# Performance work log

Measured on AMD Instinct MI355X. Metric: run time of the kernel, lower is better.

## Reference

```python
import jax, jax.numpy as jnp
import numpy as np

EMB = 2048
H = 16
Q_RANK = 1536
KV_RANK = 512
ROPE_D = 64
NOPE_D = 64
V_D = 128
QK_D = ROPE_D + NOPE_D  # 128
ROPE_BASE = 10000.0
SCALING = 1.0  # query_pre_attn_scalar ** -0.5 with scalar=1.0


def apply_rope(x):
    """torchtune-style interleaved RoPE. x: (B, S, H, D)."""
    S, D = x.shape[1], x.shape[-1]
    theta = 1.0 / (ROPE_BASE ** (jnp.arange(0, D, 2, dtype=jnp.float32) / D))  # (D/2,)
    ang = jnp.arange(S, dtype=jnp.float32)[:, None] * theta[None, :]  # (S, D/2)
    cos = jnp.cos(ang)[None, :, None, :]
    sin = jnp.sin(ang)[None, :, None, :]
    xf = x.astype(jnp.float32).reshape(*x.shape[:-1], D // 2, 2)
    x0, x1 = xf[..., 0], xf[..., 1]
    out = jnp.stack([x0 * cos - x1 * sin, x1 * cos + x0 * sin], axis=-1)
    return out.reshape(x.shape).astype(x.dtype)


def setup_inputs() -> dict:
    key = jax.random.key(0)
    ks = jax.random.split(key, 6)
    s = lambda fan_in: 1.0 / np.sqrt(fan_in)
    return {
        "x": jax.random.normal(ks[0], (2, 2048, EMB), dtype=jnp.float32),
        "q_a_w": jax.random.uniform(ks[1], (Q_RANK, EMB), jnp.float32, -s(EMB), s(EMB)),
        "q_b_w": jax.random.uniform(ks[2], (H * QK_D, Q_RANK), jnp.float32, -s(Q_RANK), s(Q_RANK)),
        "kv_a_w": jax.random.uniform(ks[3], (KV_RANK + ROPE_D, EMB), jnp.float32, -s(EMB), s(EMB)),
        "kv_b_w": jax.random.uniform(ks[4], (H * (NOPE_D + V_D), KV_RANK), jnp.float32, -s(KV_RANK), s(KV_RANK)),
        "o_w": jax.random.uniform(ks[5], (EMB, H * V_D), jnp.float32, -s(H * V_D), s(H * V_D)),
    }


def reference(x, q_a_w, q_b_w, kv_a_w, kv_b_w, o_w):
    B, S, _ = x.shape
    # LoRA-compressed Q projection
    q = (x @ q_a_w.T) @ q_b_w.T  # (B, S, H*QK_D)
    q = q.reshape(B, S, H, QK_D).transpose(0, 2, 1, 3)  # (B, H, S, QK_D)
    q_pass, q_rot = q[..., :NOPE_D], q[..., NOPE_D:]
    # Compressed KV with shared rope key
    ckv = x @ kv_a_w.T  # (B, S, KV_RANK + ROPE_D)
    k_pass_c, k_rot = ckv[..., :KV_RANK], ckv[..., KV_RANK:]
    kvb = (k_pass_c @ kv_b_w.T).reshape(B, S, H, NOPE_D + V_D).transpose(0, 2, 1, 3)
    k_pass, v = kvb[..., :NOPE_D], kvb[..., NOPE_D:]  # (B,H,S,NOPE_D), (B,H,S,V_D)
    # RoPE (applied in (B,S,H,D) layout, as in the original)
    q_rot = apply_rope(q_rot.transpose(0, 2, 1, 3)).transpose(0, 2, 1, 3)
    k_rot = apply_rope(k_rot[:, :, None, :])  # (B, S, 1, ROPE_D), shared across heads
    k_rot = jnp.broadcast_to(k_rot.transpose(0, 2, 1, 3), (B, H, S, ROPE_D))
    query = jnp.concatenate([q_pass, q_rot], axis=-1)  # (B, H, S, QK_D)
    key = jnp.concatenate([k_pass, k_rot], axis=-1)
    # NOTE: original passes attention_mask=None -> no causal mask applied.
    scores = jnp.einsum("bhqd,bhkd->bhqk", query, key) * SCALING
    attn = jax.nn.softmax(scores.astype(jnp.float32), axis=-1).astype(query.dtype)
    out = jnp.einsum("bhqk,bhkd->bhqd", attn, v)  # (B, H, S, V_D)
    out = out.transpose(0, 2, 1, 3).reshape(B, S, H * V_D)
    return out @ o_w.T
```

## Files before the change

### kernel.cpp

```cpp
#include <hip/hip_runtime.h>
#include <stdint.h>

#define EMB 2048
#define NH 16
#define QRANK 1536
#define KVRANK 512
#define ROPED 64
#define NOPED 64
#define VD 128
#define QKD 128
#define SEQ 2048
#define BATCH 2
#define BS 4096
#define BHD 32
#define NCOMB 2112
#define LOG2E 1.4426950408889634f

typedef __attribute__((ext_vector_type(4))) float f32x4;
typedef __attribute__((ext_vector_type(8))) short s16x8;
typedef __attribute__((ext_vector_type(4))) short s16x4;
typedef __attribute__((ext_vector_type(2))) unsigned int u32x2;

__device__ __forceinline__ float bf2f(unsigned short u) {
  return __uint_as_float(((unsigned int)u) << 16);
}
__device__ __forceinline__ unsigned short f2bf(float f) {
  unsigned int u = __float_as_uint(f);
  u += 0x7fff + ((u >> 16) & 1);
  return (unsigned short)(u >> 16);
}

__device__ __forceinline__ float vexp2(float x) {
#if __has_builtin(__builtin_amdgcn_exp2f)
  return __builtin_amdgcn_exp2f(x);
#else
  return exp2f(x);
#endif
}

__device__ __forceinline__ unsigned int pk_bf16_trunc(float e0, float e1) {
#if __has_builtin(__builtin_amdgcn_perm)
  return __builtin_amdgcn_perm(__float_as_uint(e1), __float_as_uint(e0), 0x07060302u);
#else
  return (__float_as_uint(e1) & 0xffff0000u) | (__float_as_uint(e0) >> 16);
#endif
}

__device__ __forceinline__ void pl32swap(unsigned int& a, unsigned int& b) {
#if __has_builtin(__builtin_amdgcn_permlane32_swap)
  u32x2 r = __builtin_amdgcn_permlane32_swap(a, b, false, false);
  a = r.x; b = r.y;
#else
  asm("v_permlane32_swap_b32 %0, %1" : "+v"(a), "+v"(b));
#endif
}
__device__ __forceinline__ void pl16swap(unsigned int& a, unsigned int& b) {
#if __has_builtin(__builtin_amdgcn_permlane16_swap)
  u32x2 r = __builtin_amdgcn_permlane16_swap(a, b, false, false);
  a = r.x; b = r.y;
#else
  asm("v_permlane16_swap_b32 %0, %1" : "+v"(a), "+v"(b));
#endif
}

__device__ __forceinline__ void gld_lds16(const unsigned short* g, unsigned short* l) {
  __builtin_amdgcn_global_load_lds((const __attribute__((address_space(1))) void*)g,
                                   (__attribute__((address_space(3))) void*)l,
                                   16, 0, 0);
}

#define N4_X   (BS * EMB / 4)
#define N4_QA  (QRANK * EMB / 4)
#define N4_KVA ((KVRANK + ROPED) * EMB / 4)
#define N4_QB  (NH * QKD * QRANK / 4)
#define N4_KVB (NH * 192 * KVRANK / 4)
#define N4_O   (EMB * NH * VD / 4)
#define N4_TOT (N4_X + N4_QA + N4_KVA + N4_QB + N4_KVB + N4_O)

__global__ void cast_all(const float* __restrict__ x, const float* __restrict__ qa,
                         const float* __restrict__ kva, const float* __restrict__ qb,
                         const float* __restrict__ kvb, const float* __restrict__ ow,
                         unsigned short* __restrict__ Xb, unsigned short* __restrict__ Wcomb,
                         unsigned short* __restrict__ Wqb, unsigned short* __restrict__ Wkvb,
                         unsigned short* __restrict__ Wo) {
  int i = blockIdx.x * blockDim.x + threadIdx.x;
  int stride = gridDim.x * blockDim.x;
  for (; i < N4_TOT; i += stride) {
    const float4* src;
    ushort4* dst;
    int j = i;
    if (j < N4_X) { src = (const float4*)x; dst = (ushort4*)Xb; }
    else if ((j -= N4_X) < N4_QA) { src = (const float4*)qa; dst = (ushort4*)Wcomb; }
    else if ((j -= N4_QA) < N4_KVA) { src = (const float4*)kva; dst = (ushort4*)(Wcomb + (size_t)QRANK * EMB); }
    else if ((j -= N4_KVA) < N4_QB) { src = (const float4*)qb; dst = (ushort4*)Wqb; }
    else if ((j -= N4_QB) < N4_KVB) { src = (const float4*)kvb; dst = (ushort4*)Wkvb; }
    else { j -= N4_KVB; src = (const float4*)ow; dst = (ushort4*)Wo; }
    float4 v = src[j];
    ushort4 o;
    o.x = f2bf(v.x); o.y = f2bf(v.y); o.z = f2bf(v.z); o.w = f2bf(v.w);
    dst[j] = o;
  }
}

template <int OUT_F32>
__global__ __launch_bounds__(256, 2) void gemm_bt(
    const unsigned short* __restrict__ A, int lda,
    const unsigned short* __restrict__ W, int ldw,
    void* __restrict__ C, int M, int N, int K)
{
  __shared__ __align__(16) unsigned short As[128 * 64];
  __shared__ __align__(16) unsigned short Ws[128 * 64];
  const int tid = threadIdx.x;
  const int wave = tid >> 6;
  const int lane = tid & 63;
  const int ln = lane & 15;
  const int quad = lane >> 4;
  const int bm = blockIdx.y * 128;
  const int bn = blockIdx.x * 128;
  const int wm = (wave >> 1) * 64;
  const int wn = (wave & 1) * 64;

  f32x4 acc[4][4] = {};

  const int rel8 = lane >> 3;
  const int csw = ((lane & 7) ^ rel8) * 8;

  for (int k0 = 0; k0 < K; k0 += 64) {
#pragma unroll
    for (int it = 0; it < 4; ++it) {
      int rb = wave * 32 + it * 8;
      gld_lds16(A + (size_t)(bm + rb + rel8) * lda + k0 + csw, &As[rb * 64]);
    }
#pragma unroll
    for (int it = 0; it < 4; ++it) {
      int rb = wave * 32 + it * 8;
      int wr = bn + rb + rel8;
      if (wr >= N) wr = N - 1;
      gld_lds16(W + (size_t)wr * ldw + k0 + csw, &Ws[rb * 64]);
    }
    __syncthreads();
#pragma unroll
    for (int kk = 0; kk < 64; kk += 32) {
      s16x8 a[4], b[4];
#pragma unroll
      for (int mt = 0; mt < 4; ++mt)
        a[mt] = *(const s16x8*)&As[(wm + mt * 16 + ln) * 64 + ((kk / 8 + quad) ^ (ln & 7)) * 8];
#pragma unroll
      for (int nt = 0; nt < 4; ++nt)
        b[nt] = *(const s16x8*)&Ws[(wn + nt * 16 + ln) * 64 + ((kk / 8 + quad) ^ (ln & 7)) * 8];
#pragma unroll
      for (int mt = 0; mt < 4; ++mt)
#pragma unroll
        for (int nt = 0; nt < 4; ++nt)
          acc[mt][nt] = __builtin_amdgcn_mfma_f32_16x16x32_bf16(a[mt], b[nt], acc[mt][nt], 0, 0, 0);
    }
    __syncthreads();
  }
#pragma unroll
  for (int mt = 0; mt < 4; ++mt) {
    int row = bm + wm + mt * 16 + quad * 4;
#pragma unroll
    for (int nt = 0; nt < 4; ++nt) {
      int col = bn + wn + nt * 16 + ln;
      if (col < N) {
#pragma unroll
        for (int r = 0; r < 4; ++r) {
          float v = acc[mt][nt][r];
          if (OUT_F32)
            ((float*)C)[(size_t)(row + r) * N + col] = v;
          else
            ((unsigned short*)C)[(size_t)(row + r) * N + col] = f2bf(v);
        }
      }
    }
  }
}

__global__ __launch_bounds__(256, 2) void gemm_q_rope(
    const unsigned short* __restrict__ A, int lda,
    const unsigned short* __restrict__ W, int ldw,
    unsigned short* __restrict__ Qry, int K)
{
  __shared__ __align__(16) unsigned short As[128 * 64];
  __shared__ __align__(16) unsigned short Ws[128 * 64];
  const int tid = threadIdx.x;
  const int wave = tid >> 6;
  const int lane = tid & 63;
  const int ln = lane & 15;
  const int quad = lane >> 4;
  const int bm = blockIdx.y * 128;
  const int bn = blockIdx.x * 128;
  const int wm = (wave >> 1) * 64;
  const int wn = (wave & 1) * 64;

  f32x4 acc[4][4] = {};
  const int rel8 = lane >> 3;
  const int csw = ((lane & 7) ^ rel8) * 8;

  for (int k0 = 0; k0 < K; k0 += 64) {
#pragma unroll
    for (int it = 0; it < 4; ++it) {
      int rb = wave * 32 + it * 8;
      gld_lds16(A + (size_t)(bm + rb + rel8) * lda + k0 + csw, &As[rb * 64]);
    }
#pragma unroll
    for (int it = 0; it < 4; ++it) {
      int rb = wave * 32 + it * 8;
      gld_lds16(W + (size_t)(bn + rb + rel8) * ldw + k0 + csw, &Ws[rb * 64]);
    }
    __syncthreads();
#pragma unroll
    for (int kk = 0; kk < 64; kk += 32) {
      s16x8 a[4], b[4];
#pragma unroll
      for (int mt = 0; mt < 4; ++mt)
        a[mt] = *(const s16x8*)&As[(wm + mt * 16 + ln) * 64 + ((kk / 8 + quad) ^ (ln & 7)) * 8];
#pragma unroll
      for (int nt = 0; nt < 4; ++nt)
        b[nt] = *(const s16x8*)&Ws[(wn + nt * 16 + ln) * 64 + ((kk / 8 + quad) ^ (ln & 7)) * 8];
#pragma unroll
      for (int mt = 0; mt < 4; ++mt)
#pragma unroll
        for (int nt = 0; nt < 4; ++nt)
          acc[mt][nt] = __builtin_amdgcn_mfma_f32_16x16x32_bf16(a[mt], b[nt], acc[mt][nt], 0, 0, 0);
    }
    __syncthreads();
  }
  const bool odd = (ln & 1);
#pragma unroll
  for (int mt = 0; mt < 4; ++mt) {
    int rowb = bm + wm + mt * 16 + quad * 4;
#pragma unroll
    for (int nt = 0; nt < 4; ++nt) {
      int col = bn + wn + nt * 16 + ln;
      int h = col >> 7, d = col & 127;
#pragma unroll
      for (int r = 0; r < 4; ++r) {
        float v = acc[mt][nt][r];
        float other = __shfl_xor(v, 1);
        int row = rowb + r;
        int b = row >> 11, s = row & 2047;
        float y = v;
        if (d >= NOPED) {
          int i = (d - NOPED) >> 1;
          float theta = exp2f(-(float)i * (13.287712379549449f / 32.f));
          float ang = (float)s * theta;
          float sn, c;
          sincosf(ang, &sn, &c);
          y = v * c + (odd ? other * sn : -other * sn);
        }
        y *= LOG2E;
        Qry[((size_t)(b * NH + h) * SEQ + s) * QKD + d] = f2bf(y);
      }
    }
  }
}

__global__ void prep_key(const unsigned short* __restrict__ kvb,
                         const unsigned short* __restrict__ cqkv,
                         unsigned short* __restrict__ Key) {
  __shared__ unsigned short krot[ROPED];
  int bs = blockIdx.x;
  int b = bs >> 11, s = bs & 2047;
  int tid = threadIdx.x;
  if (tid < 32) {
    int i = tid;
    float x0 = bf2f(cqkv[(size_t)bs * NCOMB + QRANK + KVRANK + 2 * i]);
    float x1 = bf2f(cqkv[(size_t)bs * NCOMB + QRANK + KVRANK + 2 * i + 1]);
    float theta = exp2f(-(float)i * (13.287712379549449f / 32.f));
    float ang = (float)s * theta;
    float sn, c;
    sincosf(ang, &sn, &c);
    krot[2 * i] = f2bf(x0 * c - x1 * sn);
    krot[2 * i + 1] = f2bf(x1 * c + x0 * sn);
  }
  __syncthreads();
  for (int idx = tid; idx < NH * QKD; idx += 256) {
    int h = idx >> 7, d = idx & 127;
    unsigned short v;
    if (d < NOPED)
      v = kvb[(size_t)bs * (NH * 192) + h * 192 + d];
    else
      v = krot[d - NOPED];
    Key[((size_t)(b * NH + h) * SEQ + s) * QKD + d] = v;
  }
}

__global__ void transpose_v(const unsigned short* __restrict__ kvb, unsigned short* __restrict__ VT) {
  __shared__ unsigned short tile[64][132];
  int blk = blockIdx.x;
  int bh = blk >> 5, st = blk & 31;
  int b = bh >> 4, h = bh & 15;
  int s0 = st * 64;
  int tid = threadIdx.x;
  for (int idx = tid; idx < 64 * 128; idx += 256) {
    int sl = idx >> 7, d = idx & 127;
    tile[sl][d] = kvb[((size_t)(b * SEQ + s0 + sl)) * (NH * 192) + h * 192 + NOPED + d];
  }
  __syncthreads();
  for (int idx = tid; idx < 64 * 128; idx += 256) {
    int d = idx >> 6, sl = idx & 63;
    VT[((size_t)bh * VD + d) * SEQ + s0 + sl] = tile[sl][d];
  }
}

__global__ __launch_bounds__(256, 2) void flash_attn(
    const unsigned short* __restrict__ Q,
    const unsigned short* __restrict__ Kt,
    const unsigned short* __restrict__ VT,
    unsigned short* __restrict__ O)
{
  __shared__ __align__(16) unsigned short Ks[2][64 * 128];
  __shared__ __align__(16) unsigned short Vs[2][128 * 64];

  const int tid = threadIdx.x;
  const int wave = tid >> 6;
  const int lane = tid & 63;
  const int ln = lane & 15;
  const int quad = lane >> 4;
  const int bh = blockIdx.x;
  const int q0 = blockIdx.y * 128;
  const int b = bh >> 4, h = bh & 15;

  s16x8 qa[2][4];
#pragma unroll
  for (int mt = 0; mt < 2; ++mt) {
    const unsigned short* qrow = Q + ((size_t)bh * SEQ + q0 + wave * 32 + mt * 16 + ln) * QKD;
#pragma unroll
    for (int kx = 0; kx < 4; ++kx)
      qa[mt][kx] = *(const s16x8*)(qrow + kx * 32 + quad * 8);
  }

  const int krel = lane >> 4, kcch = lane & 15;
  const int vrel8 = lane >> 3;
  const int vc8 = (lane & 7) ^ vrel8;

  auto stage = [&](int buf, int kt) {
#pragma unroll
    for (int it = 0; it < 4; ++it) {
      int rb = wave * 16 + it * 4;
      int rr = rb + krel;
      int c = kcch ^ (rr & 15);
      gld_lds16(Kt + ((size_t)bh * SEQ + kt * 64 + rr) * QKD + c * 8, &Ks[buf][rb * 128]);
    }
#pragma unroll
    for (int it = 0; it < 4; ++it) {
      int rb = wave * 32 + it * 8;
      gld_lds16(VT + ((size_t)bh * VD + rb + vrel8) * SEQ + kt * 64 + vc8 * 8, &Vs[buf][rb * 64]);
    }
  };

  f32x4 o[2][8] = {};
  float l_i[2] = {0.f, 0.f};

  stage(0, 0);

  for (int kt = 0; kt < SEQ / 64; ++kt) {
    const int cur = kt & 1;
    if (kt + 1 < SEQ / 64) {
      stage(cur ^ 1, kt + 1);
      asm volatile("s_waitcnt vmcnt(8)" ::: "memory");
    } else {
      asm volatile("s_waitcnt vmcnt(0)" ::: "memory");
    }
    asm volatile("s_barrier" ::: "memory");

    const unsigned short* Kc = Ks[cur];
    const unsigned short* Vc = Vs[cur];

    f32x4 sc[2][4];
#pragma unroll
    for (int mt = 0; mt < 2; ++mt)
#pragma unroll
      for (int t = 0; t < 4; ++t)
        sc[mt][t] = (f32x4){-20.f, -20.f, -20.f, -20.f};
    __builtin_amdgcn_s_setprio(1);
#pragma unroll
    for (int kx = 0; kx < 4; ++kx) {
      s16x8 ak[4];
#pragma unroll
      for (int t = 0; t < 4; ++t)
        ak[t] = *(const s16x8*)&Kc[(t * 16 + ln) * 128 + ((kx * 4 + quad) ^ ln) * 8];
#pragma unroll
      for (int mt = 0; mt < 2; ++mt)
#pragma unroll
        for (int t = 0; t < 4; ++t)
          sc[mt][t] = __builtin_amdgcn_mfma_f32_16x16x32_bf16(ak[t], qa[mt][kx], sc[mt][t], 0, 0, 0);
    }
    __builtin_amdgcn_s_setprio(0);

    s16x8 pfrag[2][2];
#pragma unroll
    for (int mt = 0; mt < 2; ++mt) {
      float rs = 0.f;
      unsigned int pw[4][2];
#pragma unroll
      for (int t = 0; t < 4; ++t) {
        float e0 = vexp2(sc[mt][t][0]);
        float e1 = vexp2(sc[mt][t][1]);
        float e2 = vexp2(sc[mt][t][2]);
        float e3 = vexp2(sc[mt][t][3]);
        unsigned int p01 = pk_bf16_trunc(e0, e1);
        unsigned int p23 = pk_bf16_trunc(e2, e3);
        pw[t][0] = p01; pw[t][1] = p23;
        rs += (__uint_as_float(p01 << 16) + __uint_as_float(p01 & 0xffff0000u))
            + (__uint_as_float(p23 << 16) + __uint_as_float(p23 & 0xffff0000u));
      }
      rs += __shfl_xor(rs, 16);
      rs += __shfl_xor(rs, 32);
      l_i[mt] += rs;
#pragma unroll
      for (int W = 0; W < 2; ++W) {
        unsigned int u0 = pw[2 * W][0], v0 = pw[2 * W + 1][0];
        unsigned int u1 = pw[2 * W][1], v1 = pw[2 * W + 1][1];
        pl32swap(u0, v0); pl16swap(u0, v0);
        pl32swap(u1, v1); pl16swap(u1, v1);
        union { unsigned int u[4]; s16x8 v; } fb;
        fb.u[0] = u0;
        fb.u[1] = u1;
        fb.u[2] = v0;
        fb.u[3] = v1;
        pfrag[mt][W] = fb.v;
      }
    }

    __builtin_amdgcn_s_setprio(1);
#pragma unroll
    for (int dt = 0; dt < 8; ++dt) {
      s16x8 av0 = *(const s16x8*)&Vc[(dt * 16 + ln) * 64 + ((quad ^ (ln & 7)) * 8)];
      s16x8 av1 = *(const s16x8*)&Vc[(dt * 16 + ln) * 64 + (((4 + quad) ^ (ln & 7)) * 8)];
#pragma unroll
      for (int mt = 0; mt < 2; ++mt) {
        o[mt][dt] = __builtin_amdgcn_mfma_f32_16x16x32_bf16(av0, pfrag[mt][0], o[mt][dt], 0, 0, 0);
        o[mt][dt] = __builtin_amdgcn_mfma_f32_16x16x32_bf16(av1, pfrag[mt][1], o[mt][dt], 0, 0, 0);
      }
    }
    __builtin_amdgcn_s_setprio(0);
    asm volatile("s_barrier" ::: "memory");
  }

#pragma unroll
  for (int mt = 0; mt < 2; ++mt) {
    float inv = 1.f / l_i[mt];
    int s = q0 + wave * 32 + mt * 16 + ln;
    size_t rowbase = ((size_t)b * SEQ + s) * (NH * VD) + h * VD;
#pragma unroll
    for (int dt = 0; dt < 8; ++dt) {
      ushort4 pk;
      pk.x = f2bf(o[mt][dt][0] * inv);
      pk.y = f2bf(o[mt][dt][1] * inv);
      pk.z = f2bf(o[mt][dt][2] * inv);
      pk.w = f2bf(o[mt][dt][3] * inv);
      *(ushort4*)&O[rowbase + dt * 16 + quad * 4] = pk;
    }
  }
}

extern "C" void kernel_launch(void* const* d_in, const int* in_sizes, int n_in,
                              void* d_out, int out_size, void* d_ws, size_t ws_size,
                              hipStream_t stream) {
  const float* x_f    = (const float*)d_in[0];
  const float* qaw_f  = (const float*)d_in[1];
  const float* qbw_f  = (const float*)d_in[2];
  const float* kvaw_f = (const float*)d_in[3];
  const float* kvbw_f = (const float*)d_in[4];
  const float* ow_f   = (const float*)d_in[5];

  char* ws = (char*)d_ws;
  size_t off = 0;
  auto alloc = [&](size_t n) {
    unsigned short* p = (unsigned short*)(ws + off);
    off = (off + n * 2 + 255) & ~(size_t)255;
    return p;
  };
  unsigned short* Xb    = alloc((size_t)BS * EMB);
  unsigned short* Wcomb = alloc((size_t)NCOMB * EMB);
  unsigned short* Wqb   = alloc((size_t)(NH * QKD) * QRANK);
  unsigned short* Wkvb  = alloc((size_t)(NH * 192) * KVRANK);
  unsigned short* Wo    = alloc((size_t)EMB * (NH * VD));
  unsigned short* CQKV  = alloc((size_t)BS * NCOMB);
  unsigned short* KVB   = alloc((size_t)BS * (NH * 192));
  unsigned short* Qry   = alloc((size_t)BHD * SEQ * QKD);
  unsigned short* Key   = alloc((size_t)BHD * SEQ * QKD);
  unsigned short* Vt    = alloc((size_t)BHD * VD * SEQ);
  unsigned short* AO    = alloc((size_t)BS * (NH * VD));

  cast_all<<<dim3(8192), 256, 0, stream>>>(x_f, qaw_f, kvaw_f, qbw_f, kvbw_f, ow_f,
                                           Xb, Wcomb, Wqb, Wkvb, Wo);

  gemm_bt<0><<<dim3((NCOMB + 127) / 128, BS / 128), 256, 0, stream>>>(
      Xb, EMB, Wcomb, EMB, CQKV, BS, NCOMB, EMB);
  gemm_q_rope<<<dim3((NH * QKD) / 128, BS / 128), 256, 0, stream>>>(
      CQKV, NCOMB, Wqb, QRANK, Qry, QRANK);
  gemm_bt<0><<<dim3((NH * 192) / 128, BS / 128), 256, 0, stream>>>(
      CQKV + QRANK, NCOMB, Wkvb, KVRANK, KVB, BS, NH * 192, KVRANK);

  prep_key<<<dim3(BS), 256, 0, stream>>>(KVB, CQKV, Key);
  transpose_v<<<dim3(BHD * (SEQ / 64)), 256, 0, stream>>>(KVB, Vt);

  flash_attn<<<dim3(BHD, SEQ / 128), 256, 0, stream>>>(Qry, Key, Vt, AO);

  gemm_bt<1><<<dim3(EMB / 128, BS / 128), 256, 0, stream>>>(
      AO, NH * VD, Wo, NH * VD, d_out, BS, EMB, NH * VD);
}
```

Measured before the change: 385.7 us.

## Software-pipeline flash attention: overlap QK of tile k with softmax/PV of tile k-1

Restructures the flash attention main loop so the QK^T MFMAs for the current K tile are interleaved with the exp/softmax and PV MFMAs of the previous tile, using ping-pong score registers. V staging uses triple buffering so the previous tile's V stays resident while the next one loads. The goal is to hide exp/VALU latency and LDS reads behind matrix work. In exchange it needs more LDS and more registers for a second score set, which may hurt occupancy, and it waits on all loads with vmcnt(0) at the start of each iteration.

```diff
diff --git a/kernel.cpp b/kernel.cpp
--- a/kernel.cpp
+++ b/kernel.cpp
@@ -15,6 +15,7 @@
 #define BHD 32
 #define NCOMB 2112
 #define LOG2E 1.4426950408889634f
+#define NT (SEQ / 64)
 
 typedef __attribute__((ext_vector_type(4))) float f32x4;
 typedef __attribute__((ext_vector_type(8))) short s16x8;
@@ -311,7 +312,7 @@
     unsigned short* __restrict__ O)
 {
   __shared__ __align__(16) unsigned short Ks[2][64 * 128];
-  __shared__ __align__(16) unsigned short Vs[2][128 * 64];
+  __shared__ __align__(16) unsigned short Vs[3][128 * 64];
 
   const int tid = threadIdx.x;
   const int wave = tid >> 6;
@@ -335,98 +336,78 @@
   const int vrel8 = lane >> 3;
   const int vc8 = (lane & 7) ^ vrel8;
 
-  auto stage = [&](int buf, int kt) {
+  auto stage = [&](unsigned short* Kd, unsigned short* Vd, int kt) {
 #pragma unroll
     for (int it = 0; it < 4; ++it) {
       int rb = wave * 16 + it * 4;
       int rr = rb + krel;
       int c = kcch ^ (rr & 15);
-      gld_lds16(Kt + ((size_t)bh * SEQ + kt * 64 + rr) * QKD + c * 8, &Ks[buf][rb * 128]);
+      gld_lds16(Kt + ((size_t)bh * SEQ + kt * 64 + rr) * QKD + c * 8, Kd + rb * 128);
     }
 #pragma unroll
     for (int it = 0; it < 4; ++it) {
       int rb = wave * 32 + it * 8;
-      gld_lds16(VT + ((size_t)bh * VD + rb + vrel8) * SEQ + kt * 64 + vc8 * 8, &Vs[buf][rb * 64]);
+      gld_lds16(VT + ((size_t)bh * VD + rb + vrel8) * SEQ + kt * 64 + vc8 * 8, Vd + rb * 64);
     }
   };
 
   f32x4 o[2][8] = {};
   float l_i[2] = {0.f, 0.f};
 
-  stage(0, 0);
-
-  for (int kt = 0; kt < SEQ / 64; ++kt) {
-    const int cur = kt & 1;
-    if (kt + 1 < SEQ / 64) {
-      stage(cur ^ 1, kt + 1);
-      asm volatile("s_waitcnt vmcnt(8)" ::: "memory");
-    } else {
-      asm volatile("s_waitcnt vmcnt(0)" ::: "memory");
-    }
-    asm volatile("s_barrier" ::: "memory");
-
-    const unsigned short* Kc = Ks[cur];
-    const unsigned short* Vc = Vs[cur];
-
-    f32x4 sc[2][4];
+  auto sc_init = [&](f32x4 (&sc)[2][4]) {
 #pragma unroll
     for (int mt = 0; mt < 2; ++mt)
 #pragma unroll
       for (int t = 0; t < 4; ++t)
         sc[mt][t] = (f32x4){-20.f, -20.f, -20.f, -20.f};
-    __builtin_amdgcn_s_setprio(1);
-#pragma unroll
-    for (int kx = 0; kx < 4; ++kx) {
-      s16x8 ak[4];
+  };
+  auto qk_kx = [&](int kx, const unsigned short* Kc, f32x4 (&sc)[2][4]) {
+    s16x8 ak[4];
+#pragma unroll
+    for (int t = 0; t < 4; ++t)
+      ak[t] = *(const s16x8*)&Kc[(t * 16 + ln) * 128 + ((kx * 4 + quad) ^ ln) * 8];
+#pragma unroll
+    for (int mt = 0; mt < 2; ++mt)
 #pragma unroll
       for (int t = 0; t < 4; ++t)
-        ak[t] = *(const s16x8*)&Kc[(t * 16 + ln) * 128 + ((kx * 4 + quad) ^ ln) * 8];
-#pragma unroll
-      for (int mt = 0; mt < 2; ++mt)
-#pragma unroll
-        for (int t = 0; t < 4; ++t)
-          sc[mt][t] = __builtin_amdgcn_mfma_f32_16x16x32_bf16(ak[t], qa[mt][kx], sc[mt][t], 0, 0, 0);
-    }
-    __builtin_amdgcn_s_setprio(0);
-
-    s16x8 pfrag[2][2];
-#pragma unroll
-    for (int mt = 0; mt < 2; ++mt) {
-      float rs = 0.f;
-      unsigned int pw[4][2];
-#pragma unroll
-      for (int t = 0; t < 4; ++t) {
-        float e0 = vexp2(sc[mt][t][0]);
-        float e1 = vexp2(sc[mt][t][1]);
-        float e2 = vexp2(sc[mt][t][2]);
-        float e3 = vexp2(sc[mt][t][3]);
-        unsigned int p01 = pk_bf16_trunc(e0, e1);
-        unsigned int p23 = pk_bf16_trunc(e2, e3);
-        pw[t][0] = p01; pw[t][1] = p23;
-        rs += (__uint_as_float(p01 << 16) + __uint_as_float(p01 & 0xffff0000u))
-            + (__uint_as_float(p23 << 16) + __uint_as_float(p23 & 0xffff0000u));
-      }
-      rs += __shfl_xor(rs, 16);
-      rs += __shfl_xor(rs, 32);
-      l_i[mt] += rs;
-#pragma unroll
-      for (int W = 0; W < 2; ++W) {
-        unsigned int u0 = pw[2 * W][0], v0 = pw[2 * W + 1][0];
-        unsigned int u1 = pw[2 * W][1], v1 = pw[2 * W + 1][1];
-        pl32swap(u0, v0); pl16swap(u0, v0);
-        pl32swap(u1, v1); pl16swap(u1, v1);
-        union { unsigned int u[4]; s16x8 v; } fb;
-        fb.u[0] = u0;
-        fb.u[1] = u1;
-        fb.u[2] = v0;
-        fb.u[3] = v1;
-        pfrag[mt][W] = fb.v;
-      }
-    }
-
-    __builtin_amdgcn_s_setprio(1);
-#pragma unroll
-    for (int dt = 0; dt < 8; ++dt) {
+        sc[mt][t] = __builtin_amdgcn_mfma_f32_16x16x32_bf16(ak[t], qa[mt][kx], sc[mt][t], 0, 0, 0);
+  };
+  auto sm_mt = [&](int mt, f32x4 (&sc)[2][4], s16x8 (&pfrag)[2][2]) {
+    float rs = 0.f;
+    unsigned int pw[4][2];
+#pragma unroll
+    for (int t = 0; t < 4; ++t) {
+      float e0 = vexp2(sc[mt][t][0]);
+      float e1 = vexp2(sc[mt][t][1]);
+      float e2 = vexp2(sc[mt][t][2]);
+      float e3 = vexp2(sc[mt][t][3]);
+      unsigned int p01 = pk_bf16_trunc(e0, e1);
+      unsigned int p23 = pk_bf16_trunc(e2, e3);
+      pw[t][0] = p01; pw[t][1] = p23;
+      rs += (__uint_as_float(p01 << 16) + __uint_as_float(p01 & 0xffff0000u))
+          + (__uint_as_float(p23 << 16) + __uint_as_float(p23 & 0xffff0000u));
+    }
+    rs += __shfl_xor(rs, 16);
+    rs += __shfl_xor(rs, 32);
+    l_i[mt] += rs;
+#pragma unroll
+    for (int W = 0; W < 2; ++W) {
+      unsigned int u0 = pw[2 * W][0], v0 = pw[2 * W + 1][0];
+      unsigned int u1 = pw[2 * W][1], v1 = pw[2 * W + 1][1];
+      pl32swap(u0, v0); pl16swap(u0, v0);
+      pl32swap(u1, v1); pl16swap(u1, v1);
+      union { unsigned int u[4]; s16x8 v; } fb;
+      fb.u[0] = u0;
+      fb.u[1] = u1;
+      fb.u[2] = v0;
+      fb.u[3] = v1;
+      pfrag[mt][W] = fb.v;
+    }
+  };
+  auto pv_half = [&](int half, const unsigned short* Vc, s16x8 (&pfrag)[2][2]) {
+#pragma unroll
+    for (int dd = 0; dd < 4; ++dd) {
+      int dt = half * 4 + dd;
       s16x8 av0 = *(const s16x8*)&Vc[(dt * 16 + ln) * 64 + ((quad ^ (ln & 7)) * 8)];
       s16x8 av1 = *(const s16x8*)&Vc[(dt * 16 + ln) * 64 + (((4 + quad) ^ (ln & 7)) * 8)];
 #pragma unroll
@@ -435,8 +416,57 @@
         o[mt][dt] = __builtin_amdgcn_mfma_f32_16x16x32_bf16(av1, pfrag[mt][1], o[mt][dt], 0, 0, 0);
       }
     }
+  };
+
+  auto iter = [&](int kt, f32x4 (&scP)[2][4], f32x4 (&scC)[2][4]) {
+    asm volatile("s_waitcnt vmcnt(0)" ::: "memory");
+    asm volatile("s_barrier" ::: "memory");
+    if (kt + 1 < NT)
+      stage(Ks[(kt + 1) & 1], Vs[(kt + 1) % 3], kt + 1);
+    const unsigned short* Kc = Ks[kt & 1];
+    const unsigned short* Vp = Vs[(kt - 1) % 3];
+    s16x8 pfrag[2][2];
+    __builtin_amdgcn_s_setprio(1);
+    sc_init(scC);
+    qk_kx(0, Kc, scC);
+    sm_mt(0, scP, pfrag);
+    qk_kx(1, Kc, scC);
+    sm_mt(1, scP, pfrag);
+    qk_kx(2, Kc, scC);
+    pv_half(0, Vp, pfrag);
+    qk_kx(3, Kc, scC);
+    pv_half(1, Vp, pfrag);
     __builtin_amdgcn_s_setprio(0);
-    asm volatile("s_barrier" ::: "memory");
+  };
+
+  f32x4 scA[2][4], scB[2][4];
+
+  stage(Ks[0], Vs[0], 0);
+  asm volatile("s_waitcnt vmcnt(0)" ::: "memory");
+  asm volatile("s_barrier" ::: "memory");
+  stage(Ks[1], Vs[1], 1);
+  __builtin_amdgcn_s_setprio(1);
+  sc_init(scA);
+  qk_kx(0, Ks[0], scA);
+  qk_kx(1, Ks[0], scA);
+  qk_kx(2, Ks[0], scA);
+  qk_kx(3, Ks[0], scA);
+  __builtin_amdgcn_s_setprio(0);
+
+  int kt = 1;
+#pragma unroll 1
+  for (int p = 0; p < 15; ++p, kt += 2) {
+    iter(kt, scA, scB);
+    iter(kt + 1, scB, scA);
+  }
+  iter(31, scA, scB);
+
+  {
+    s16x8 pfrag[2][2];
+    sm_mt(0, scB, pfrag);
+    sm_mt(1, scB, pfrag);
+    pv_half(0, Vs[1], pfrag);
+    pv_half(1, Vs[1], pfrag);
   }
 
 #pragma unroll
```

New measurement: 386.5 us. No clear change (+0.2%).

## Fuse key prep with V transpose and single-buffer K to raise attention occupancy

Applied to the files above, without the earlier changes.

Merges the prep_key and transpose_v kernels into one prep_kv kernel that builds the rotated key and transposed V per (head, 64-row) tile, with vectorised V loads. This removes a launch and one extra pass over KVB. In flash_attn, K goes from double to single buffering: the next K tile is loaded after a barrier that follows QK^T, while V stays double-buffered. The freed LDS lets launch bounds rise from 2 to 3 blocks per SM. The price is an extra barrier per iteration and less room to hide K load latency.

```diff
diff --git a/kernel.cpp b/kernel.cpp
--- a/kernel.cpp
+++ b/kernel.cpp
@@ -15,6 +15,7 @@
 #define BHD 32
 #define NCOMB 2112
 #define LOG2E 1.4426950408889634f
+#define NT (SEQ / 64)
 
 typedef __attribute__((ext_vector_type(4))) float f32x4;
 typedef __attribute__((ext_vector_type(8))) short s16x8;
@@ -256,61 +257,59 @@
   }
 }
 
-__global__ void prep_key(const unsigned short* __restrict__ kvb,
-                         const unsigned short* __restrict__ cqkv,
-                         unsigned short* __restrict__ Key) {
-  __shared__ unsigned short krot[ROPED];
-  int bs = blockIdx.x;
-  int b = bs >> 11, s = bs & 2047;
-  int tid = threadIdx.x;
-  if (tid < 32) {
-    int i = tid;
-    float x0 = bf2f(cqkv[(size_t)bs * NCOMB + QRANK + KVRANK + 2 * i]);
-    float x1 = bf2f(cqkv[(size_t)bs * NCOMB + QRANK + KVRANK + 2 * i + 1]);
-    float theta = exp2f(-(float)i * (13.287712379549449f / 32.f));
-    float ang = (float)s * theta;
-    float sn, c;
-    sincosf(ang, &sn, &c);
-    krot[2 * i] = f2bf(x0 * c - x1 * sn);
-    krot[2 * i + 1] = f2bf(x1 * c + x0 * sn);
-  }
-  __syncthreads();
-  for (int idx = tid; idx < NH * QKD; idx += 256) {
-    int h = idx >> 7, d = idx & 127;
-    unsigned short v;
-    if (d < NOPED)
-      v = kvb[(size_t)bs * (NH * 192) + h * 192 + d];
-    else
-      v = krot[d - NOPED];
-    Key[((size_t)(b * NH + h) * SEQ + s) * QKD + d] = v;
-  }
-}
-
-__global__ void transpose_v(const unsigned short* __restrict__ kvb, unsigned short* __restrict__ VT) {
-  __shared__ unsigned short tile[64][132];
+__global__ void prep_kv(const unsigned short* __restrict__ kvb,
+                        const unsigned short* __restrict__ cqkv,
+                        unsigned short* __restrict__ Key,
+                        unsigned short* __restrict__ VT) {
+  __shared__ unsigned short vt[64][132];
+  __shared__ unsigned short kr[64][64];
   int blk = blockIdx.x;
   int bh = blk >> 5, st = blk & 31;
   int b = bh >> 4, h = bh & 15;
   int s0 = st * 64;
   int tid = threadIdx.x;
+
+  for (int idx = tid; idx < 64 * 32; idx += 256) {
+    int sl = idx >> 5, i = idx & 31;
+    int s = s0 + sl;
+    const unsigned short* rp = cqkv + (size_t)(b * SEQ + s) * NCOMB + QRANK + KVRANK;
+    float x0 = bf2f(rp[2 * i]);
+    float x1 = bf2f(rp[2 * i + 1]);
+    float theta = exp2f(-(float)i * (13.287712379549449f / 32.f));
+    float ang = (float)s * theta;
+    float sn, c;
+    sincosf(ang, &sn, &c);
+    kr[sl][2 * i] = f2bf(x0 * c - x1 * sn);
+    kr[sl][2 * i + 1] = f2bf(x1 * c + x0 * sn);
+  }
+  for (int idx = tid; idx < 64 * 16; idx += 256) {
+    int sl = idx >> 4, dc = idx & 15;
+    s16x8 v = *(const s16x8*)(kvb + (size_t)(b * SEQ + s0 + sl) * (NH * 192) + h * 192 + NOPED + dc * 8);
+    *(s16x8*)&vt[sl][dc * 8] = v;
+  }
+  __syncthreads();
   for (int idx = tid; idx < 64 * 128; idx += 256) {
     int sl = idx >> 7, d = idx & 127;
-    tile[sl][d] = kvb[((size_t)(b * SEQ + s0 + sl)) * (NH * 192) + h * 192 + NOPED + d];
-  }
-  __syncthreads();
+    unsigned short v;
+    if (d < NOPED)
+      v = kvb[(size_t)(b * SEQ + s0 + sl) * (NH * 192) + h * 192 + d];
+    else
+      v = kr[sl][d - NOPED];
+    Key[((size_t)bh * SEQ + s0 + sl) * QKD + d] = v;
+  }
   for (int idx = tid; idx < 64 * 128; idx += 256) {
     int d = idx >> 6, sl = idx & 63;
-    VT[((size_t)bh * VD + d) * SEQ + s0 + sl] = tile[sl][d];
-  }
-}
-
-__global__ __launch_bounds__(256, 2) void flash_attn(
+    VT[((size_t)bh * VD + d) * SEQ + s0 + sl] = vt[sl][d];
+  }
+}
+
+__global__ __launch_bounds__(256, 3) void flash_attn(
     const unsigned short* __restrict__ Q,
     const unsigned short* __restrict__ Kt,
     const unsigned short* __restrict__ VT,
     unsigned short* __restrict__ O)
 {
-  __shared__ __align__(16) unsigned short Ks[2][64 * 128];
+  __shared__ __align__(16) unsigned short Ks[64 * 128];
   __shared__ __align__(16) unsigned short Vs[2][128 * 64];
 
   const int tid = threadIdx.x;
@@ -335,14 +334,16 @@
   const int vrel8 = lane >> 3;
   const int vc8 = (lane & 7) ^ vrel8;
 
-  auto stage = [&](int buf, int kt) {
+  auto stage_k = [&](int kt) {
 #pragma unroll
     for (int it = 0; it < 4; ++it) {
       int rb = wave * 16 + it * 4;
       int rr = rb + krel;
       int c = kcch ^ (rr & 15);
-      gld_lds16(Kt + ((size_t)bh * SEQ + kt * 64 + rr) * QKD + c * 8, &Ks[buf][rb * 128]);
-    }
+      gld_lds16(Kt + ((size_t)bh * SEQ + kt * 64 + rr) * QKD + c * 8, &Ks[rb * 128]);
+    }
+  };
+  auto stage_v = [&](int buf, int kt) {
 #pragma unroll
     for (int it = 0; it < 4; ++it) {
       int rb = wave * 32 + it * 8;
@@ -353,20 +354,14 @@
   f32x4 o[2][8] = {};
   float l_i[2] = {0.f, 0.f};
 
-  stage(0, 0);
-
-  for (int kt = 0; kt < SEQ / 64; ++kt) {
-    const int cur = kt & 1;
-    if (kt + 1 < SEQ / 64) {
-      stage(cur ^ 1, kt + 1);
-      asm volatile("s_waitcnt vmcnt(8)" ::: "memory");
-    } else {
-      asm volatile("s_waitcnt vmcnt(0)" ::: "memory");
-    }
-    asm volatile("s_barrier" ::: "memory");
-
-    const unsigned short* Kc = Ks[cur];
-    const unsigned short* Vc = Vs[cur];
+  stage_k(0);
+  stage_v(0, 0);
+  asm volatile("s_waitcnt vmcnt(0)" ::: "memory");
+  asm volatile("s_barrier" ::: "memory");
+
+  for (int kt = 0; kt < NT; ++kt) {
+    if (kt + 1 < NT)
+      stage_v((kt + 1) & 1, kt + 1);
 
     f32x4 sc[2][4];
 #pragma unroll
@@ -380,7 +375,7 @@
       s16x8 ak[4];
 #pragma unroll
       for (int t = 0; t < 4; ++t)
-        ak[t] = *(const s16x8*)&Kc[(t * 16 + ln) * 128 + ((kx * 4 + quad) ^ ln) * 8];
+        ak[t] = *(const s16x8*)&Ks[(t * 16 + ln) * 128 + ((kx * 4 + quad) ^ ln) * 8];
 #pragma unroll
       for (int mt = 0; mt < 2; ++mt)
 #pragma unroll
@@ -388,6 +383,10 @@
           sc[mt][t] = __builtin_amdgcn_mfma_f32_16x16x32_bf16(ak[t], qa[mt][kx], sc[mt][t], 0, 0, 0);
     }
     __builtin_amdgcn_s_setprio(0);
+
+    asm volatile("s_barrier" ::: "memory");
+    if (kt + 1 < NT)
+      stage_k(kt + 1);
 
     s16x8 pfrag[2][2];
 #pragma unroll
@@ -424,6 +423,7 @@
       }
     }
 
+    const unsigned short* Vc = Vs[kt & 1];
     __builtin_amdgcn_s_setprio(1);
 #pragma unroll
     for (int dt = 0; dt < 8; ++dt) {
@@ -436,6 +436,8 @@
       }
     }
     __builtin_amdgcn_s_setprio(0);
+
+    asm volatile("s_waitcnt vmcnt(0)" ::: "memory");
     asm volatile("s_barrier" ::: "memory");
   }
 
@@ -495,8 +497,7 @@
   gemm_bt<0><<<dim3((NH * 192) / 128, BS / 128), 256, 0, stream>>>(
       CQKV + QRANK, NCOMB, Wkvb, KVRANK, KVB, BS, NH * 192, KVRANK);
 
-  prep_key<<<dim3(BS), 256, 0, stream>>>(KVB, CQKV, Key);
-  transpose_v<<<dim3(BHD * (SEQ / 64)), 256, 0, stream>>>(KVB, Vt);
+  prep_kv<<<dim3(BHD * (SEQ / 64)), 256, 0, stream>>>(KVB, CQKV, Key, Vt);
 
   flash_attn<<<dim3(BHD, SEQ / 128), 256, 0, stream>>>(Qry, Key, Vt, AO);
 
```

Result: slower. 407.3 us (+5.6%).
